# Performance work log

Measured on AMD Instinct MI355X. Metric: run time of the kernel, lower is better.

The kernel has to match this reference:

```python
import jax, jax.numpy as jnp
import numpy as np

N = 50000          # nodes
E = 600000         # edges
D = 128            # g_dim = h1_dim = h2_dim
R = 8              # 2 * n_speakers**2, n_speakers=2
B = 10             # num_bases


def setup_inputs() -> dict:
    key = jax.random.key(0)
    ks = jax.random.split(key, 10)
    s = 1.0 / np.sqrt(D)
    return {
        "node_features": jax.random.normal(ks[0], (N, D), jnp.float32),
        "edge_index": jax.random.randint(ks[1], (2, E), 0, N, jnp.int64),
        "edge_type": jax.random.randint(ks[2], (E,), 0, R, jnp.int64),
        # RGCNConv params (basis decomposition)
        "basis": jax.random.normal(ks[3], (B, D, D), jnp.float32) * s,
        "comp": jax.random.normal(ks[4], (R, B), jnp.float32) * (1.0 / np.sqrt(B)),
        "root": jax.random.normal(ks[5], (D, D), jnp.float32) * s,
        "bias1": jnp.zeros((D,), jnp.float32),
        # GraphConv params
        "w_rel": jax.random.normal(ks[6], (D, D), jnp.float32) * s,
        "b_rel": jnp.zeros((D,), jnp.float32),
        "w_root": jax.random.normal(ks[7], (D, D), jnp.float32) * s,
    }


def reference(node_features, edge_index, edge_type, basis, comp, root, bias1, w_rel, b_rel, w_root):
    x = node_features
    n = x.shape[0]
    r = comp.shape[0]
    src, dst = edge_index[0], edge_index[1]

    # ---- RGCNConv (basis decomposition, per-relation mean aggregation) ----
    # project through bases once: [N, B, D]
    xb = jnp.einsum('ni,bio->nbo', x, basis)
    # per-edge message: combine bases with relation coefficients  [E, D]
    msg = jnp.einsum('eb,ebo->eo', comp[edge_type], xb[src])
    # per-(dst, relation) mean normalization
    seg = dst * r + edge_type                       # [E]
    cnt = jax.ops.segment_sum(jnp.ones((msg.shape[0],), x.dtype), seg, num_segments=n * r)
    norm = 1.0 / jnp.maximum(cnt[seg], 1.0)         # [E]
    agg = jax.ops.segment_sum(msg * norm[:, None], dst, num_segments=n)  # [N, D]
    h1 = agg + x @ root + bias1

    # ---- GraphConv (add aggregation of neighbors + root transform) ----
    nbr = jax.ops.segment_sum(h1[src], dst, num_segments=n)  # [N, D]
    out = nbr @ w_rel.T + b_rel + h1 @ w_root.T
    return out
```

## Files before the change

### kernel.cpp

```cpp
#include <hip/hip_runtime.h>
#include <stdint.h>

#define N_NODES 50000
#define E_EDGES 600000
#define D 128
#define R_REL 8
#define B_BASES 10
#define RN (R_REL * N_NODES)

typedef __attribute__((ext_vector_type(8))) short bf16x8;
typedef __attribute__((ext_vector_type(4))) float f32x4;

__device__ __forceinline__ short f2b(float f) {
    uint32_t u = __float_as_uint(f);
    u += 0x7fff + ((u >> 16) & 1);
    return (short)(u >> 16);
}
__device__ __forceinline__ float b2f(uint16_t u) {
    return __uint_as_float((uint32_t)u << 16);
}

__global__ __launch_bounds__(256) void k_front(const float* __restrict__ x,
                                               unsigned short* __restrict__ xb,
                                               const int* __restrict__ dst,
                                               const int* __restrict__ et,
                                               int* __restrict__ cntr,
                                               const float* __restrict__ basis,
                                               const float* __restrict__ comp,
                                               const float* __restrict__ root,
                                               const float* __restrict__ wrel,
                                               const float* __restrict__ wroot,
                                               short* __restrict__ wt,
                                               short* __restrict__ wrel_b,
                                               short* __restrict__ wroot_b) {
    const int XB_N = N_NODES * D / 8;
    int tid = blockIdx.x * 256 + threadIdx.x;
    if (tid < XB_N) {
        const float4* s = (const float4*)x + (size_t)tid * 2;
        float4 v0 = s[0], v1 = s[1];
        union { uint4 u; unsigned short h[8]; } pk;
        pk.h[0] = (unsigned short)f2b(v0.x); pk.h[1] = (unsigned short)f2b(v0.y);
        pk.h[2] = (unsigned short)f2b(v0.z); pk.h[3] = (unsigned short)f2b(v0.w);
        pk.h[4] = (unsigned short)f2b(v1.x); pk.h[5] = (unsigned short)f2b(v1.y);
        pk.h[6] = (unsigned short)f2b(v1.z); pk.h[7] = (unsigned short)f2b(v1.w);
        ((uint4*)xb)[tid] = pk.u;
    } else if (tid < XB_N + E_EDGES) {
        int e = tid - XB_N;
        atomicAdd(&cntr[dst[e] * R_REL + et[e]], 1);
    } else {
        int t2 = tid - XB_N - E_EDGES;
        if (t2 < 9 * D * D) {
            int s = t2 >> 14;
            int rem = t2 & 16383;
            int j = rem >> 7, i = rem & 127;
            float v;
            if (s < 8) {
                v = 0.f;
#pragma unroll
                for (int b = 0; b < B_BASES; b++)
                    v += comp[s * B_BASES + b] * basis[b * D * D + i * D + j];
            } else {
                v = root[i * D + j];
            }
            wt[t2] = f2b(v);
        } else {
            int t3 = t2 - 9 * D * D;
            if (t3 < D * D) {
                wrel_b[t3]  = f2b(wrel[t3]);
                wroot_b[t3] = f2b(wroot[t3]);
            }
        }
    }
}

__device__ __forceinline__ int wave_scan_incl(int v) {
    int lane = threadIdx.x & 63;
#pragma unroll
    for (int off = 1; off < 64; off <<= 1) {
        int n = __shfl_up(v, off, 64);
        if (lane >= off) v += n;
    }
    return v;
}

__global__ __launch_bounds__(1024) void k_scan_a(const int* __restrict__ in,
                                                 int* __restrict__ out,
                                                 int* __restrict__ bsum, int n) {
    __shared__ int wsum[16];
    int t = threadIdx.x, lane = t & 63, wid = t >> 6;
    int g = blockIdx.x * 1024 + t;
    int v = (g < n) ? in[g] : 0;
    int isc = wave_scan_incl(v);
    if (lane == 63) wsum[wid] = isc;
    __syncthreads();
    if (wid == 0) {
        int wv = (lane < 16) ? wsum[lane] : 0;
        int wsc = wave_scan_incl(wv);
        if (lane < 16) wsum[lane] = wsc - wv;
    }
    __syncthreads();
    if (g < n) out[g] = wsum[wid] + isc - v;
    if (t == 1023 && bsum) bsum[blockIdx.x] = wsum[15] + isc;
}

__global__ __launch_bounds__(1024) void k_scan_c(int* __restrict__ out,
                                                 const int* __restrict__ bsum, int n) {
    int g = blockIdx.x * 1024 + threadIdx.x;
    if (g < n) out[g] += bsum[blockIdx.x];
}

__global__ __launch_bounds__(256) void k_bucket(const int* __restrict__ src,
                                                const int* __restrict__ dst,
                                                const int* __restrict__ et,
                                                int* __restrict__ seg_off,
                                                int* __restrict__ es1) {
    int e = blockIdx.x * 256 + threadIdx.x;
    if (e >= E_EDGES) return;
    int key = dst[e] * R_REL + et[e];
    int pos = atomicAdd(&seg_off[key], 1);
    es1[pos] = src[e];
}

__global__ __launch_bounds__(256) void k_aggmean(const unsigned short* __restrict__ xb,
                                                 const int* __restrict__ es1,
                                                 const int* __restrict__ seg_off,
                                                 unsigned short* __restrict__ mx) {
    int t = threadIdx.x;
    int sw = t >> 4, l = t & 15;
    int k = blockIdx.x * 16 + sw;
    if (k >= RN) return;
    int start = (k == 0) ? 0 : seg_off[k - 1];
    int end = seg_off[k];
    float ax[8];
#pragma unroll
    for (int q = 0; q < 8; q++) ax[q] = 0.f;
    size_t loff = (size_t)l * 8;
    int pos = start;
    for (; pos + 2 <= end; pos += 2) {
        int s0 = es1[pos], s1 = es1[pos + 1];
        uint4 v0 = *(const uint4*)(xb + (size_t)s0 * D + loff);
        uint4 v1 = *(const uint4*)(xb + (size_t)s1 * D + loff);
        const uint32_t* w0 = (const uint32_t*)&v0;
        const uint32_t* w1 = (const uint32_t*)&v1;
#pragma unroll
        for (int q = 0; q < 4; q++) {
            ax[q * 2]     += b2f((uint16_t)w0[q]) + b2f((uint16_t)w1[q]);
            ax[q * 2 + 1] += b2f((uint16_t)(w0[q] >> 16)) + b2f((uint16_t)(w1[q] >> 16));
        }
    }
    if (pos < end) {
        int s0 = es1[pos];
        uint4 v0 = *(const uint4*)(xb + (size_t)s0 * D + loff);
        const uint32_t* w0 = (const uint32_t*)&v0;
#pragma unroll
        for (int q = 0; q < 4; q++) {
            ax[q * 2]     += b2f((uint16_t)w0[q]);
            ax[q * 2 + 1] += b2f((uint16_t)(w0[q] >> 16));
        }
    }
    float nm = (end > start) ? 1.f / (float)(end - start) : 0.f;
    union { uint4 u; unsigned short h[8]; } pk;
#pragma unroll
    for (int q = 0; q < 8; q++) pk.h[q] = (unsigned short)f2b(ax[q] * nm);
    size_t krow = (size_t)(k & 7) * N_NODES + (size_t)(k >> 3);
    *(uint4*)(mx + krow * D + loff) = pk.u;
}

__global__ __launch_bounds__(256, 3) void k_h1_gemm(const unsigned short* __restrict__ mxall,
                                                    const short* __restrict__ wt,
                                                    const float* __restrict__ bias1,
                                                    unsigned short* __restrict__ h1b) {
    __shared__ short ws[128 * 128];
    int t = threadIdx.x;
    int wave = t >> 6, lane = t & 63, quad = lane >> 4, l16 = lane & 15;
    int base = blockIdx.x * 64;
    int n0 = base + wave * 16 + l16;
    int nc0 = n0 < N_NODES ? n0 : N_NODES - 1;
    int ci0 = wave * 8;

    uint4 aReg[2][4];
    uint4 wn[8];

#pragma unroll
    for (int i = 0; i < 8; i++) {
        int row = (ci0 + i) * 4 + quad;
        wn[i] = *(const uint4*)(wt + row * D + (l16 << 3));
    }
#pragma unroll
    for (int kc = 0; kc < 4; kc++) {
        int co = (kc * 4 + quad) * 8;
        aReg[0][kc] = *(const uint4*)(mxall + ((size_t)0 * N_NODES + nc0) * D + co);
        aReg[1][kc] = *(const uint4*)(mxall + ((size_t)1 * N_NODES + nc0) * D + co);
    }
#pragma unroll
    for (int i = 0; i < 8; i++) {
        int row = (ci0 + i) * 4 + quad;
        *(uint4*)&ws[row * 128 + ((l16 ^ (row & 15)) << 3)] = wn[i];
    }
    __syncthreads();

    f32x4 acc[8];
#pragma unroll
    for (int jt = 0; jt < 8; jt++) acc[jt] = (f32x4){0.f, 0.f, 0.f, 0.f};

#pragma unroll
    for (int s = 0; s < 9; s++) {
        const int par = s & 1;
        bf16x8 a[4];
#pragma unroll
        for (int kc = 0; kc < 4; kc++) a[kc] = *(bf16x8*)&aReg[par][kc];
        if (s + 2 < 9) {
#pragma unroll
            for (int kc = 0; kc < 4; kc++) {
                int co = (kc * 4 + quad) * 8;
                aReg[par][kc] = *(const uint4*)(mxall + ((size_t)(s + 2) * N_NODES + nc0) * D + co);
            }
        }
        if (s + 1 < 9) {
            const short* wb = wt + (size_t)(s + 1) * D * D;
#pragma unroll
            for (int i = 0; i < 8; i++) {
                int row = (ci0 + i) * 4 + quad;
                wn[i] = *(const uint4*)(wb + row * D + (l16 << 3));
            }
        }
#pragma unroll
        for (int kc = 0; kc < 4; kc++) {
            int c0 = kc * 4 + quad;
#pragma unroll
            for (int jt = 0; jt < 8; jt++) {
                bf16x8 b = *(const bf16x8*)&ws[(jt * 16 + l16) * 128 + ((c0 ^ l16) << 3)];
                acc[jt] = __builtin_amdgcn_mfma_f32_16x16x32_bf16(a[kc], b, acc[jt], 0, 0, 0);
            }
        }
        if (s + 1 < 9) {
            __syncthreads();
#pragma unroll
            for (int i = 0; i < 8; i++) {
                int row = (ci0 + i) * 4 + quad;
                *(uint4*)&ws[row * 128 + ((l16 ^ (row & 15)) << 3)] = wn[i];
            }
            __syncthreads();
        }
    }

#pragma unroll
    for (int reg = 0; reg < 4; reg++) {
        int node = base + wave * 16 + quad * 4 + reg;
        if (node >= N_NODES) continue;
#pragma unroll
        for (int jt = 0; jt < 8; jt++) {
            int col = jt * 16 + l16;
            float v = acc[jt][reg] + bias1[col];
            h1b[(size_t)node * D + col] = (unsigned short)f2b(v);
        }
    }
}

__global__ __launch_bounds__(256) void k_agg_nbr(const unsigned short* __restrict__ h1b,
                                                 const int* __restrict__ es1,
                                                 const int* __restrict__ seg_off,
                                                 unsigned short* __restrict__ nbr) {
    int t = threadIdx.x;
    int wave = t >> 6, lane = t & 63, sub = lane >> 4, l = lane & 15;
    int d = blockIdx.x * 16 + wave * 4 + sub;
    if (d >= N_NODES) return;
    int start = (d == 0) ? 0 : seg_off[d * R_REL - 1];
    int end = seg_off[d * R_REL + 7];
    float acc[8];
#pragma unroll
    for (int j = 0; j < 8; j++) acc[j] = 0.f;
    size_t loff = (size_t)l * 8;

    int pos = start;
    for (; pos + 4 <= end; pos += 4) {
        int i0 = es1[pos], i1 = es1[pos + 1], i2 = es1[pos + 2], i3 = es1[pos + 3];
        uint4 v0 = *(const uint4*)(h1b + (size_t)i0 * D + loff);
        uint4 v1 = *(const uint4*)(h1b + (size_t)i1 * D + loff);
        uint4 v2 = *(const uint4*)(h1b + (size_t)i2 * D + loff);
        uint4 v3 = *(const uint4*)(h1b + (size_t)i3 * D + loff);
        const uint32_t* w0 = (const uint32_t*)&v0;
        const uint32_t* w1 = (const uint32_t*)&v1;
        const uint32_t* w2 = (const uint32_t*)&v2;
        const uint32_t* w3 = (const uint32_t*)&v3;
#pragma unroll
        for (int q = 0; q < 4; q++) {
            acc[q * 2]     += b2f((uint16_t)w0[q]) + b2f((uint16_t)w1[q]) +
                              b2f((uint16_t)w2[q]) + b2f((uint16_t)w3[q]);
            acc[q * 2 + 1] += b2f((uint16_t)(w0[q] >> 16)) + b2f((uint16_t)(w1[q] >> 16)) +
                              b2f((uint16_t)(w2[q] >> 16)) + b2f((uint16_t)(w3[q] >> 16));
        }
    }
    for (; pos < end; pos++) {
        int i0 = es1[pos];
        uint4 v0 = *(const uint4*)(h1b + (size_t)i0 * D + loff);
        const uint32_t* w0 = (const uint32_t*)&v0;
#pragma unroll
        for (int q = 0; q < 4; q++) {
            acc[q * 2]     += b2f((uint16_t)w0[q]);
            acc[q * 2 + 1] += b2f((uint16_t)(w0[q] >> 16));
        }
    }

    union { uint4 u; unsigned short h[8]; } pk;
#pragma unroll
    for (int j = 0; j < 8; j++) pk.h[j] = (unsigned short)f2b(acc[j]);
    *(uint4*)(nbr + (size_t)d * D + loff) = pk.u;
}

__global__ __launch_bounds__(256) void k_out2(const unsigned short* __restrict__ h1b,
                                              const unsigned short* __restrict__ nbr,
                                              const short* __restrict__ wroot_b,
                                              const short* __restrict__ wrel_b,
                                              const float* __restrict__ brel,
                                              float* __restrict__ out) {
    __shared__ short ws[2][128 * 128];
    int t = threadIdx.x;
    int wave = t >> 6, lane = t & 63, quad = lane >> 4, l16 = lane & 15;
    int base = blockIdx.x * 128;
    int n0 = base + wave * 32 + l16;
    int n1 = n0 + 16;
    int nc0 = n0 < N_NODES ? n0 : N_NODES - 1;
    int nc1 = n1 < N_NODES ? n1 : N_NODES - 1;
    int ci0 = wave * 8;

    uint4 aReg[2][2][4];
    {
        uint4 b0[8];
#pragma unroll
        for (int i = 0; i < 8; i++) {
            int row = (ci0 + i) * 4 + quad;
            b0[i] = *(const uint4*)(wroot_b + row * D + (l16 << 3));
        }
#pragma unroll
        for (int kc = 0; kc < 4; kc++) {
            int co = (kc * 4 + quad) * 8;
            aReg[0][0][kc] = *(const uint4*)(h1b + (size_t)nc0 * D + co);
            aReg[0][1][kc] = *(const uint4*)(h1b + (size_t)nc1 * D + co);
            aReg[1][0][kc] = *(const uint4*)(nbr + (size_t)nc0 * D + co);
            aReg[1][1][kc] = *(const uint4*)(nbr + (size_t)nc1 * D + co);
        }
#pragma unroll
        for (int i = 0; i < 8; i++) {
            int row = (ci0 + i) * 4 + quad;
            *(uint4*)&ws[0][row * 128 + ((l16 ^ (row & 15)) << 3)] = b0[i];
        }
    }
    __syncthreads();

    f32x4 acc[2][8];
#pragma unroll
    for (int tl = 0; tl < 2; tl++)
#pragma unroll
        for (int jt = 0; jt < 8; jt++) acc[tl][jt] = (f32x4){0.f, 0.f, 0.f, 0.f};

#pragma unroll
    for (int s = 0; s < 2; s++) {
        int cur = s & 1;
        uint4 bn[8];
        if (s == 0) {
#pragma unroll
            for (int i = 0; i < 8; i++) {
                int row = (ci0 + i) * 4 + quad;
                bn[i] = *(const uint4*)(wrel_b + row * D + (l16 << 3));
            }
        }
#pragma unroll
        for (int kc = 0; kc < 4; kc++) {
            int c0 = kc * 4 + quad;
            bf16x8 a0 = *(bf16x8*)&aReg[cur][0][kc];
            bf16x8 a1 = *(bf16x8*)&aReg[cur][1][kc];
#pragma unroll
            for (int jt = 0; jt < 8; jt++) {
                bf16x8 b = *(const bf16x8*)&ws[cur][(jt * 16 + l16) * 128 + ((c0 ^ l16) << 3)];
                acc[0][jt] = __builtin_amdgcn_mfma_f32_16x16x32_bf16(a0, b, acc[0][jt], 0, 0, 0);
                acc[1][jt] = __builtin_amdgcn_mfma_f32_16x16x32_bf16(a1, b, acc[1][jt], 0, 0, 0);
            }
        }
        if (s == 0) {
#pragma unroll
            for (int i = 0; i < 8; i++) {
                int row = (ci0 + i) * 4 + quad;
                *(uint4*)&ws[1][row * 128 + ((l16 ^ (row & 15)) << 3)] = bn[i];
            }
            __syncthreads();
        }
    }

#pragma unroll
    for (int tl = 0; tl < 2; tl++) {
#pragma unroll
        for (int reg = 0; reg < 4; reg++) {
            int node = base + wave * 32 + tl * 16 + quad * 4 + reg;
            if (node >= N_NODES) continue;
#pragma unroll
            for (int jt = 0; jt < 8; jt++) {
                int col = jt * 16 + l16;
                out[(size_t)node * D + col] = acc[tl][jt][reg] + brel[col];
            }
        }
    }
}

extern "C" void kernel_launch(void* const* d_in, const int* in_sizes, int n_in,
                              void* d_out, int out_size, void* d_ws, size_t ws_size,
                              hipStream_t stream) {
    const float* x     = (const float*)d_in[0];
    const int*   ei    = (const int*)d_in[1];
    const int*   et    = (const int*)d_in[2];
    const float* basis = (const float*)d_in[3];
    const float* comp  = (const float*)d_in[4];
    const float* root  = (const float*)d_in[5];
    const float* bias1 = (const float*)d_in[6];
    const float* wrel  = (const float*)d_in[7];
    const float* brel  = (const float*)d_in[8];
    const float* wroot = (const float*)d_in[9];
    float* out = (float*)d_out;
    const int* src = ei;
    const int* dst = ei + E_EDGES;

    char* p = (char*)d_ws;
    auto alloc = [&](size_t bytes) { char* q = p; p += (bytes + 255) & ~(size_t)255; return q; };
    short* wt      = (short*)alloc((size_t)9 * D * D * sizeof(short));
    short* wrel_b  = (short*)alloc(D * D * sizeof(short));
    short* wroot_b = (short*)alloc(D * D * sizeof(short));
    int*   cntr    = (int*)alloc((size_t)RN * sizeof(int));
    int*   seg_off = (int*)alloc((size_t)RN * sizeof(int));
    int*   es1     = (int*)alloc((size_t)(E_EDGES + 16) * sizeof(int));
    int*   bsum    = (int*)alloc(1024 * sizeof(int));
    unsigned short* mxall = (unsigned short*)alloc((size_t)9 * N_NODES * D * sizeof(unsigned short));
    unsigned short* h1b   = (unsigned short*)alloc((size_t)N_NODES * D * sizeof(unsigned short));
    unsigned short* xb  = mxall + (size_t)8 * N_NODES * D;
    unsigned short* mx  = mxall;
    unsigned short* nbr = mxall;

    hipMemsetAsync(cntr, 0, (size_t)RN * sizeof(int), stream);

    const int XB_N = N_NODES * D / 8;
    int nfront = (XB_N + E_EDGES + 9 * D * D + D * D + 255) / 256;
    k_front<<<nfront, 256, 0, stream>>>(x, xb, dst, et, cntr,
                                        basis, comp, root, wrel, wroot,
                                        wt, wrel_b, wroot_b);

    int nscan = (RN + 1023) / 1024;
    k_scan_a<<<nscan, 1024, 0, stream>>>(cntr, seg_off, bsum, RN);
    k_scan_a<<<1, 1024, 0, stream>>>(bsum, bsum, nullptr, nscan);
    k_scan_c<<<nscan, 1024, 0, stream>>>(seg_off, bsum, RN);

    k_bucket<<<(E_EDGES + 255) / 256, 256, 0, stream>>>(src, dst, et, seg_off, es1);

    k_aggmean<<<RN / 16, 256, 0, stream>>>(xb, es1, seg_off, mx);

    int nbh = (N_NODES + 63) / 64;
    int nb2 = (N_NODES + 127) / 128;
    int na = (N_NODES + 15) / 16;
    k_h1_gemm<<<nbh, 256, 0, stream>>>(mxall, wt, bias1, h1b);
    k_agg_nbr<<<na, 256, 0, stream>>>(h1b, es1, seg_off, nbr);
    k_out2<<<nb2, 256, 0, stream>>>(h1b, nbr, wroot_b, wrel_b, brel, out);
}
```

Measured before the change: 328.4 us.

## Fuse per-relation mean aggregation into the RGCN GEMM kernel

Removes the separate aggregation kernel and computes each node's per-relation mean of bf16 basis-projected rows directly inside the GEMM, building the MFMA A-fragments in registers. This eliminates writing and rereading a large 8xNxD intermediate buffer and one kernel launch. In exchange, the irregular gather now sits inside the GEMM loop without prefetching, with divergence across lanes of differing degree and higher register pressure.

```diff
diff --git a/kernel.cpp b/kernel.cpp
--- a/kernel.cpp
+++ b/kernel.cpp
@@ -121,78 +121,38 @@
     es1[pos] = src[e];
 }
 
-__global__ __launch_bounds__(256) void k_aggmean(const unsigned short* __restrict__ xb,
-                                                 const int* __restrict__ es1,
-                                                 const int* __restrict__ seg_off,
-                                                 unsigned short* __restrict__ mx) {
-    int t = threadIdx.x;
-    int sw = t >> 4, l = t & 15;
-    int k = blockIdx.x * 16 + sw;
-    if (k >= RN) return;
-    int start = (k == 0) ? 0 : seg_off[k - 1];
-    int end = seg_off[k];
-    float ax[8];
-#pragma unroll
-    for (int q = 0; q < 8; q++) ax[q] = 0.f;
-    size_t loff = (size_t)l * 8;
-    int pos = start;
-    for (; pos + 2 <= end; pos += 2) {
-        int s0 = es1[pos], s1 = es1[pos + 1];
-        uint4 v0 = *(const uint4*)(xb + (size_t)s0 * D + loff);
-        uint4 v1 = *(const uint4*)(xb + (size_t)s1 * D + loff);
-        const uint32_t* w0 = (const uint32_t*)&v0;
-        const uint32_t* w1 = (const uint32_t*)&v1;
-#pragma unroll
-        for (int q = 0; q < 4; q++) {
-            ax[q * 2]     += b2f((uint16_t)w0[q]) + b2f((uint16_t)w1[q]);
-            ax[q * 2 + 1] += b2f((uint16_t)(w0[q] >> 16)) + b2f((uint16_t)(w1[q] >> 16));
-        }
-    }
-    if (pos < end) {
-        int s0 = es1[pos];
-        uint4 v0 = *(const uint4*)(xb + (size_t)s0 * D + loff);
-        const uint32_t* w0 = (const uint32_t*)&v0;
-#pragma unroll
-        for (int q = 0; q < 4; q++) {
-            ax[q * 2]     += b2f((uint16_t)w0[q]);
-            ax[q * 2 + 1] += b2f((uint16_t)(w0[q] >> 16));
-        }
-    }
-    float nm = (end > start) ? 1.f / (float)(end - start) : 0.f;
-    union { uint4 u; unsigned short h[8]; } pk;
-#pragma unroll
-    for (int q = 0; q < 8; q++) pk.h[q] = (unsigned short)f2b(ax[q] * nm);
-    size_t krow = (size_t)(k & 7) * N_NODES + (size_t)(k >> 3);
-    *(uint4*)(mx + krow * D + loff) = pk.u;
-}
-
-__global__ __launch_bounds__(256, 3) void k_h1_gemm(const unsigned short* __restrict__ mxall,
-                                                    const short* __restrict__ wt,
-                                                    const float* __restrict__ bias1,
-                                                    unsigned short* __restrict__ h1b) {
+__global__ __launch_bounds__(256, 3) void k_h1_fused(const unsigned short* __restrict__ xb,
+                                                     const int* __restrict__ es1,
+                                                     const int* __restrict__ seg_off,
+                                                     const short* __restrict__ wt,
+                                                     const float* __restrict__ bias1,
+                                                     unsigned short* __restrict__ h1b) {
     __shared__ short ws[128 * 128];
     int t = threadIdx.x;
     int wave = t >> 6, lane = t & 63, quad = lane >> 4, l16 = lane & 15;
     int base = blockIdx.x * 64;
     int n0 = base + wave * 16 + l16;
-    int nc0 = n0 < N_NODES ? n0 : N_NODES - 1;
+    bool nvalid = n0 < N_NODES;
+    int nc0 = nvalid ? n0 : N_NODES - 1;
     int ci0 = wave * 8;
 
-    uint4 aReg[2][4];
+    int b[9];
+    {
+        int k0 = n0 * R_REL;
+#pragma unroll
+        for (int i = 0; i < 9; i++) {
+            int idx = k0 - 1 + i;
+            b[i] = (nvalid && idx >= 0) ? seg_off[idx] : 0;
+        }
+    }
+
     uint4 wn[8];
-
 #pragma unroll
     for (int i = 0; i < 8; i++) {
         int row = (ci0 + i) * 4 + quad;
         wn[i] = *(const uint4*)(wt + row * D + (l16 << 3));
     }
 #pragma unroll
-    for (int kc = 0; kc < 4; kc++) {
-        int co = (kc * 4 + quad) * 8;
-        aReg[0][kc] = *(const uint4*)(mxall + ((size_t)0 * N_NODES + nc0) * D + co);
-        aReg[1][kc] = *(const uint4*)(mxall + ((size_t)1 * N_NODES + nc0) * D + co);
-    }
-#pragma unroll
     for (int i = 0; i < 8; i++) {
         int row = (ci0 + i) * 4 + quad;
         *(uint4*)&ws[row * 128 + ((l16 ^ (row & 15)) << 3)] = wn[i];
@@ -203,19 +163,10 @@
 #pragma unroll
     for (int jt = 0; jt < 8; jt++) acc[jt] = (f32x4){0.f, 0.f, 0.f, 0.f};
 
+    const unsigned short* xrow_q = xb + (size_t)quad * 8;
+
 #pragma unroll
     for (int s = 0; s < 9; s++) {
-        const int par = s & 1;
-        bf16x8 a[4];
-#pragma unroll
-        for (int kc = 0; kc < 4; kc++) a[kc] = *(bf16x8*)&aReg[par][kc];
-        if (s + 2 < 9) {
-#pragma unroll
-            for (int kc = 0; kc < 4; kc++) {
-                int co = (kc * 4 + quad) * 8;
-                aReg[par][kc] = *(const uint4*)(mxall + ((size_t)(s + 2) * N_NODES + nc0) * D + co);
-            }
-        }
         if (s + 1 < 9) {
             const short* wb = wt + (size_t)(s + 1) * D * D;
 #pragma unroll
@@ -224,15 +175,53 @@
                 wn[i] = *(const uint4*)(wb + row * D + (l16 << 3));
             }
         }
+
+        bf16x8 afrag[4];
+        if (s < 8) {
+            float m[4][8];
+#pragma unroll
+            for (int kc = 0; kc < 4; kc++)
+#pragma unroll
+                for (int q = 0; q < 8; q++) m[kc][q] = 0.f;
+            int start = b[s], end = b[s + 1];
+            for (int pos = start; pos < end; ++pos) {
+                int srow = es1[pos];
+                const unsigned short* rp = xrow_q + (size_t)srow * D;
+#pragma unroll
+                for (int kc = 0; kc < 4; kc++) {
+                    uint4 g = *(const uint4*)(rp + kc * 32);
+                    const uint32_t* w = (const uint32_t*)&g;
+#pragma unroll
+                    for (int q = 0; q < 4; q++) {
+                        m[kc][q * 2]     += b2f((uint16_t)w[q]);
+                        m[kc][q * 2 + 1] += b2f((uint16_t)(w[q] >> 16));
+                    }
+                }
+            }
+            float nm = (end > start) ? 1.f / (float)(end - start) : 0.f;
+#pragma unroll
+            for (int kc = 0; kc < 4; kc++) {
+                union { uint4 u; unsigned short h[8]; } pk;
+#pragma unroll
+                for (int q = 0; q < 8; q++) pk.h[q] = (unsigned short)f2b(m[kc][q] * nm);
+                afrag[kc] = *(bf16x8*)&pk.u;
+            }
+        } else {
+#pragma unroll
+            for (int kc = 0; kc < 4; kc++)
+                afrag[kc] = *(const bf16x8*)(xb + (size_t)nc0 * D + kc * 32 + quad * 8);
+        }
+
 #pragma unroll
         for (int kc = 0; kc < 4; kc++) {
             int c0 = kc * 4 + quad;
 #pragma unroll
             for (int jt = 0; jt < 8; jt++) {
-                bf16x8 b = *(const bf16x8*)&ws[(jt * 16 + l16) * 128 + ((c0 ^ l16) << 3)];
-                acc[jt] = __builtin_amdgcn_mfma_f32_16x16x32_bf16(a[kc], b, acc[jt], 0, 0, 0);
-            }
-        }
+                bf16x8 bb = *(const bf16x8*)&ws[(jt * 16 + l16) * 128 + ((c0 ^ l16) << 3)];
+                acc[jt] = __builtin_amdgcn_mfma_f32_16x16x32_bf16(afrag[kc], bb, acc[jt], 0, 0, 0);
+            }
+        }
+
         if (s + 1 < 9) {
             __syncthreads();
 #pragma unroll
@@ -428,11 +417,9 @@
     int*   seg_off = (int*)alloc((size_t)RN * sizeof(int));
     int*   es1     = (int*)alloc((size_t)(E_EDGES + 16) * sizeof(int));
     int*   bsum    = (int*)alloc(1024 * sizeof(int));
-    unsigned short* mxall = (unsigned short*)alloc((size_t)9 * N_NODES * D * sizeof(unsigned short));
-    unsigned short* h1b   = (unsigned short*)alloc((size_t)N_NODES * D * sizeof(unsigned short));
-    unsigned short* xb  = mxall + (size_t)8 * N_NODES * D;
-    unsigned short* mx  = mxall;
-    unsigned short* nbr = mxall;
+    unsigned short* xb  = (unsigned short*)alloc((size_t)N_NODES * D * sizeof(unsigned short));
+    unsigned short* h1b = (unsigned short*)alloc((size_t)N_NODES * D * sizeof(unsigned short));
+    unsigned short* nbr = xb;
 
     hipMemsetAsync(cntr, 0, (size_t)RN * sizeof(int), stream);
 
@@ -449,12 +436,10 @@
 
     k_bucket<<<(E_EDGES + 255) / 256, 256, 0, stream>>>(src, dst, et, seg_off, es1);
 
-    k_aggmean<<<RN / 16, 256, 0, stream>>>(xb, es1, seg_off, mx);
-
     int nbh = (N_NODES + 63) / 64;
     int nb2 = (N_NODES + 127) / 128;
     int na = (N_NODES + 15) / 16;
-    k_h1_gemm<<<nbh, 256, 0, stream>>>(mxall, wt, bias1, h1b);
+    k_h1_fused<<<nbh, 256, 0, stream>>>(xb, es1, seg_off, wt, bias1, h1b);
     k_agg_nbr<<<na, 256, 0, stream>>>(h1b, es1, seg_off, nbr);
     k_out2<<<nb2, 256, 0, stream>>>(h1b, nbr, wroot_b, wrel_b, brel, out);
 }
```

Result: slower. 366.3 us (+11.6%).
